# Kernel tuning notes

Measured on AMD Instinct MI355X. Metric: run time of the kernel, lower is better.

## Reference

```python
import jax, jax.numpy as jnp
import numpy as np

EMB = 256   # EMB_SIZE hard-coded in source
H = 8       # num heads (all heads share the same Q/K/V, as in source)
DK = EMB // H  # 32
B, T = 16, 2048
LN_EPS = 1e-5


def _layernorm(a, g, b):
    m = jnp.mean(a, axis=-1, keepdims=True)
    v = jnp.mean(jnp.square(a - m), axis=-1, keepdims=True)
    return (a - m) * jax.lax.rsqrt(v + LN_EPS) * g + b


def setup_inputs() -> dict:
    key = jax.random.key(0)
    ks = jax.random.split(key, 8)
    sc = 0.02
    return {
        "x": jax.random.normal(ks[0], (B, T, EMB), jnp.float32),
        "Wq": jax.random.normal(ks[1], (EMB, DK), jnp.float32) * sc,
        "Wk": jax.random.normal(ks[2], (EMB, DK), jnp.float32) * sc,
        "Wv": jax.random.normal(ks[3], (EMB, DK), jnp.float32) * sc,
        "Wp": jax.random.normal(ks[4], (EMB, EMB), jnp.float32) * sc,
        "bp": jnp.zeros((EMB,), jnp.float32),
        "W1": jax.random.normal(ks[5], (EMB, 4 * EMB), jnp.float32) * sc,
        "b1": jnp.zeros((4 * EMB,), jnp.float32),
        "W2": jax.random.normal(ks[6], (4 * EMB, EMB), jnp.float32) * sc,
        "b2": jnp.zeros((EMB,), jnp.float32),
        "g1": jnp.ones((EMB,), jnp.float32),
        "be1": jnp.zeros((EMB,), jnp.float32),
        "g2": jnp.ones((EMB,), jnp.float32),
        "be2": jnp.zeros((EMB,), jnp.float32),
    }


def reference(x, Wq, Wk, Wv, Wp, bp, W1, b1, W2, b2, g1, be1, g2, be2):
    # Single shared-head QKV projections (bias-free), as in source
    q = x @ Wq  # [B,T,DK]
    k = x @ Wk
    v = x @ Wv
    # Causal self-attention with explicit score matrix [B,T,T]
    scores = jnp.einsum("btd,bsd->bts", q, k) / jnp.sqrt(jnp.float32(DK))
    causal = jnp.tril(jnp.ones((T, T), dtype=bool))
    scores = jnp.where(causal, scores, -jnp.inf)
    a = jax.nn.softmax(scores, axis=-1)
    attn = jnp.einsum("bts,bsd->btd", a, v)  # [B,T,DK]
    # Source concatenates h identical copies of the same attention output
    cat = jnp.tile(attn, (1, 1, H))  # [B,T,EMB]
    mh = cat @ Wp + bp
    y1 = _layernorm(x + mh, g1, be1)
    ff = jax.nn.gelu(y1 @ W1 + b1, approximate=False) @ W2 + b2
    return _layernorm(y1 + ff, g2, be2)
```

## Files before the change

### kernel.cpp

```cpp
#include <hip/hip_runtime.h>

#define BB 16
#define TT 2048
#define EE 256
#define DK 32
#define MM (BB*TT)
#define FF 1024

typedef __bf16 bf16_t;
typedef __bf16 bf16x8 __attribute__((ext_vector_type(8)));
typedef __bf16 bf16x4 __attribute__((ext_vector_type(4)));
typedef float  f32x4  __attribute__((ext_vector_type(4)));

__device__ __forceinline__ f32x4 mfma16(bf16x8 a, bf16x8 b, f32x4 c){
  return __builtin_amdgcn_mfma_f32_16x16x32_bf16(a, b, c, 0, 0, 0);
}
__device__ __forceinline__ void gload_lds16(const void* g, void* l){
  __builtin_amdgcn_global_load_lds((__attribute__((address_space(1))) void*)g,
                                   (__attribute__((address_space(3))) void*)l,
                                   16, 0, 0);
}

__launch_bounds__(256)
__global__ void prep_kernel(const float* __restrict__ Wq, const float* __restrict__ Wk,
                            const float* __restrict__ Wv, const float* __restrict__ Wp,
                            const float* __restrict__ W1, const float* __restrict__ W2,
                            bf16_t* __restrict__ wqkv, bf16_t* __restrict__ wpT,
                            bf16_t* __restrict__ w1t, bf16_t* __restrict__ w2t)
{
  const int i = blockIdx.x*256 + threadIdx.x;
  if (i < 96*256) {
    const int r = i >> 8, c = i & 255;
    float v;
    if (r < 32)      v = Wq[c*32 + r] * 0.17677669529663687f;
    else if (r < 64) v = Wk[c*32 + (r-32)];
    else             v = Wv[c*32 + (r-64)];
    wqkv[i] = (bf16_t)v;
  }
  if (i < 256*32) {
    const int n = i >> 5, k = i & 31;
    float s = 0.f;
    #pragma unroll
    for (int h = 0; h < 8; ++h) s += Wp[(h*32 + k)*256 + n];
    wpT[i] = (bf16_t)s;
  }
  if (i < 1024*256) {
    const int n = i >> 8, k = i & 255;
    w1t[i] = (bf16_t)W1[(size_t)k*1024 + n];
  }
  if (i < 256*1024) {
    const int n = i >> 10, k = i & 1023;
    w2t[i] = (bf16_t)W2[(size_t)k*256 + n];
  }
}

__launch_bounds__(256)
__global__ void qkv_kernel(const float* __restrict__ x, const bf16_t* __restrict__ wqkv,
                           bf16_t* __restrict__ q, bf16_t* __restrict__ kd,
                           bf16_t* __restrict__ vT)
{
  __shared__ bf16_t Ws[96*256];
  bf16_t* Vt = Ws;
  const int tid = threadIdx.x;
  #pragma unroll
  for (int i = 0; i < 12; ++i) {
    const int v8  = tid + i*256;
    const int row = v8 >> 5;
    const int bir = (v8 & 31) * 16;
    *(bf16x8*)((char*)Ws + row*512 + (bir ^ ((row & 7) << 4))) =
        *(const bf16x8*)(wqkv + (size_t)v8*8);
  }
  __syncthreads();

  const int w = tid >> 6, l = tid & 63;
  const int lr = l & 15, lk4 = l >> 4, lkb = lk4*8;
  const int m0 = blockIdx.x * 64;
  const int arow = m0 + w*16 + lr;
  const float* xr = x + (size_t)arow * 256;

  f32x4 acc[6] = {};
  #pragma unroll
  for (int s = 0; s < 8; ++s) {
    const int kb = s*32 + lkb;
    const float4 v0 = *(const float4*)(xr + kb);
    const float4 v1 = *(const float4*)(xr + kb + 4);
    bf16x8 a;
    a[0]=(bf16_t)v0.x; a[1]=(bf16_t)v0.y; a[2]=(bf16_t)v0.z; a[3]=(bf16_t)v0.w;
    a[4]=(bf16_t)v1.x; a[5]=(bf16_t)v1.y; a[6]=(bf16_t)v1.z; a[7]=(bf16_t)v1.w;
    #pragma unroll
    for (int j = 0; j < 6; ++j) {
      const int nrow = j*16 + lr;
      const bf16x8 bf = *(const bf16x8*)((const char*)Ws + nrow*512 +
                                         ((kb*2) ^ ((nrow & 7) << 4)));
      acc[j] = mfma16(a, bf, acc[j]);
    }
  }
  #pragma unroll
  for (int j = 0; j < 4; ++j) {
    #pragma unroll
    for (int r = 0; r < 4; ++r) {
      const int orow = m0 + w*16 + lk4*4 + r;
      const int col  = j*16 + lr;
      const bf16_t v = (bf16_t)acc[j][r];
      if (col < 32) q[(size_t)orow*32 + col] = v;
      else          kd[(size_t)orow*32 + (col-32)] = v;
    }
  }
  __syncthreads();
  #pragma unroll
  for (int j = 4; j < 6; ++j)
    #pragma unroll
    for (int r = 0; r < 4; ++r) {
      const int d = (j-4)*16 + lr;
      const int t = w*16 + lk4*4 + r;
      *(bf16_t*)((char*)Vt + d*128 + ((((t>>3) ^ (d&7))<<4) | ((t&7)*2))) =
          (bf16_t)acc[j][r];
    }
  __syncthreads();
  {
    const int d = tid >> 3, c8 = tid & 7;
    const bf16x8 v = *(const bf16x8*)((char*)Vt + d*128 + ((c8 ^ (d&7))<<4));
    *(bf16x8*)(vT + ((size_t)(m0 >> 11)*32 + d)*TT + (m0 & 2047) + c8*8) = v;
  }
}

__launch_bounds__(256)
__global__ void attnp_kernel(const bf16_t* __restrict__ q, const bf16_t* __restrict__ kd,
                             const bf16_t* __restrict__ vT,
                             float* __restrict__ part_acc, float* __restrict__ part_ml)
{
  __shared__ bf16_t P[4][16*128];
  const int tid = threadIdx.x;
  const int w = tid >> 6, l = tid & 63;
  const int wv = blockIdx.x*4 + w;
  const int lr = l & 15, g4 = l >> 4;
  const float NEG_INF = -__builtin_inff();

  const int b = wv / 320;
  const int u = wv - b*320;
  int r, base;
  if      (u >= 192) { r = 3; base = 192; }
  else if (u >= 96)  { r = 2; base = 96;  }
  else if (u >= 32)  { r = 1; base = 32;  }
  else               { r = 0; base = 0;   }
  const int qq = u - base;
  const int g  = r*32 + qq / (r+1);
  const int c  = qq - (qq / (r+1))*(r+1);
  const int t_total = (g >> 3) + 1;
  const int t0 = c*4;
  const int t1 = min(t0 + 4, t_total);

  const bf16_t* qb = q  + (size_t)b*TT*32;
  const bf16_t* kb = kd + (size_t)b*TT*32;
  const bf16_t* vb = vT + (size_t)b*32*TT;
  const int q0 = g*16;
  const int qg = q0 + lr;

  const bf16x8 qa = *(const bf16x8*)(qb + (size_t)(q0 + lr)*32 + g4*8);
  const bf16_t* v0r = vb + (size_t)lr*TT;
  const bf16_t* v1r = vb + (size_t)(16 + lr)*TT;

  f32x4 acc0 = {0.f,0.f,0.f,0.f}, acc1 = {0.f,0.f,0.f,0.f};
  float mrun = NEG_INF, lsum = 0.f;
  char* pb = (char*)&P[w][0];
  const int swz = (lr & 7) << 4;
  const f32x4 zf = {0.f,0.f,0.f,0.f};

  for (int t = t0; t < t1; ++t) {
    const int k0 = t * 128;
    f32x4 s[8];
    #pragma unroll
    for (int cc = 0; cc < 8; ++cc) {
      const bf16x8 kf = *(const bf16x8*)(kb + (size_t)(k0 + cc*16 + lr)*32 + g4*8);
      s[cc] = mfma16(kf, qa, zf);
    }
    if (t == t_total - 1) {
      #pragma unroll
      for (int cc = 0; cc < 8; ++cc)
        #pragma unroll
        for (int rr = 0; rr < 4; ++rr)
          if (k0 + cc*16 + g4*4 + rr > qg) s[cc][rr] = NEG_INF;
    }
    float mt = NEG_INF;
    #pragma unroll
    for (int cc = 0; cc < 8; ++cc) {
      float a01 = fmaxf(s[cc][0], s[cc][1]), a23 = fmaxf(s[cc][2], s[cc][3]);
      mt = fmaxf(mt, fmaxf(a01, a23));
    }
    mt = fmaxf(mt, __shfl_xor(mt, 16));
    mt = fmaxf(mt, __shfl_xor(mt, 32));
    const float mn = fmaxf(mrun, mt);
    const float sc = __expf(mrun - mn);
    float ps = 0.f;
    #pragma unroll
    for (int cc = 0; cc < 8; ++cc) {
      float p0 = __expf(s[cc][0]-mn), p1 = __expf(s[cc][1]-mn);
      float p2 = __expf(s[cc][2]-mn), p3 = __expf(s[cc][3]-mn);
      s[cc][0]=p0; s[cc][1]=p1; s[cc][2]=p2; s[cc][3]=p3;
      ps += (p0+p1) + (p2+p3);
    }
    ps += __shfl_xor(ps, 16);
    ps += __shfl_xor(ps, 32);
    lsum = lsum*sc + ps;
    mrun = mn;
    acc0 *= sc; acc1 *= sc;
    #pragma unroll
    for (int cc = 0; cc < 8; ++cc) {
      bf16x4 pk;
      pk[0]=(bf16_t)s[cc][0]; pk[1]=(bf16_t)s[cc][1];
      pk[2]=(bf16_t)s[cc][2]; pk[3]=(bf16_t)s[cc][3];
      *(bf16x4*)(pb + lr*256 + ((cc*32 + g4*8) ^ swz)) = pk;
    }
    #pragma unroll
    for (int h = 0; h < 4; ++h) {
      const bf16x8 pbf = *(const bf16x8*)(pb + lr*256 + ((h*64 + g4*16) ^ swz));
      acc0 = mfma16(*(const bf16x8*)(v0r + k0 + h*32 + g4*8), pbf, acc0);
      acc1 = mfma16(*(const bf16x8*)(v1r + k0 + h*32 + g4*8), pbf, acc1);
    }
  }
  float* pa = part_acc + (size_t)wv*512;
  *(f32x4*)(pa + l*8)     = acc0;
  *(f32x4*)(pa + l*8 + 4) = acc1;
  if (l < 16) {
    part_ml[wv*32 + l]      = mrun;
    part_ml[wv*32 + 16 + l] = lsum;
  }
}

__launch_bounds__(256)
__global__ void ln1f_kernel(const float* __restrict__ part_acc,
                            const float* __restrict__ part_ml,
                            const bf16_t* __restrict__ wpT,
                            const float* __restrict__ bp, const float* __restrict__ x,
                            const float* __restrict__ g1, const float* __restrict__ be1,
                            bf16_t* __restrict__ y1b)
{
  __shared__ char SM[57344];
  char* wp_s  = SM;
  char* att_s = SM + 16384;
  float* bp_s = (float*)(SM + 20480);
  char* y_s   = SM + 24576;
  const int tid = threadIdx.x;
  const int w = tid >> 6, l = tid & 63;
  const int lr = l & 15, g4 = l >> 4;
  const float NEG_INF = -__builtin_inff();

  #pragma unroll
  for (int p = 0; p < 4; ++p) {
    const int idx = p*256 + tid;
    const int n = idx >> 2, c = idx & 3;
    gload_lds16(wpT + (size_t)n*32 + ((c ^ (n & 3)) * 8), wp_s + idx*16);
  }
  if (tid < 64) ((float4*)bp_s)[tid] = ((const float4*)bp)[tid];

  const int id = blockIdx.x*4 + w;
  const int b = id >> 7, g = id & 127;
  {
    const int rr = g >> 5;
    const int base = (rr == 0) ? 0 : (rr == 1) ? 32 : (rr == 2) ? 96 : 192;
    const int p0 = b*320 + base + (g - (rr << 5))*(rr + 1);
    const int nc = rr + 1;
    float M = NEG_INF;
    float mv0=NEG_INF, mv1=NEG_INF, mv2=NEG_INF, mv3=NEG_INF;
    float lv0=0, lv1=0, lv2=0, lv3=0;
    f32x4 a00={0,0,0,0}, a01={0,0,0,0}, a10={0,0,0,0}, a11={0,0,0,0};
    f32x4 a20={0,0,0,0}, a21={0,0,0,0}, a30={0,0,0,0}, a31={0,0,0,0};
    {
      const float* pa = part_acc + (size_t)p0*512;
      a00 = *(const f32x4*)(pa + l*8); a01 = *(const f32x4*)(pa + l*8 + 4);
      mv0 = part_ml[p0*32 + lr]; lv0 = part_ml[p0*32 + 16 + lr];
    }
    if (nc > 1) {
      const float* pa = part_acc + (size_t)(p0+1)*512;
      a10 = *(const f32x4*)(pa + l*8); a11 = *(const f32x4*)(pa + l*8 + 4);
      mv1 = part_ml[(p0+1)*32 + lr]; lv1 = part_ml[(p0+1)*32 + 16 + lr];
    }
    if (nc > 2) {
      const float* pa = part_acc + (size_t)(p0+2)*512;
      a20 = *(const f32x4*)(pa + l*8); a21 = *(const f32x4*)(pa + l*8 + 4);
      mv2 = part_ml[(p0+2)*32 + lr]; lv2 = part_ml[(p0+2)*32 + 16 + lr];
    }
    if (nc > 3) {
      const float* pa = part_acc + (size_t)(p0+3)*512;
      a30 = *(const f32x4*)(pa + l*8); a31 = *(const f32x4*)(pa + l*8 + 4);
      mv3 = part_ml[(p0+3)*32 + lr]; lv3 = part_ml[(p0+3)*32 + 16 + lr];
    }
    M = fmaxf(fmaxf(mv0, mv1), fmaxf(mv2, mv3));
    const float w0 = __expf(mv0 - M), w1 = __expf(mv1 - M);
    const float w2 = __expf(mv2 - M), w3 = __expf(mv3 - M);
    const float L = lv0*w0 + lv1*w1 + lv2*w2 + lv3*w3;
    const float inv = 1.0f / L;
    const f32x4 o0 = (a00*w0 + a10*w1 + a20*w2 + a30*w3) * inv;
    const f32x4 o1 = (a01*w0 + a11*w1 + a21*w2 + a31*w3) * inv;
    char* ab = att_s + w*1024;
    bf16x4 h0, h1;
    #pragma unroll
    for (int r = 0; r < 4; ++r) { h0[r] = (bf16_t)o0[r]; h1[r] = (bf16_t)o1[r]; }
    *(bf16x4*)(ab + lr*64 + ((g4*8)      ^ ((lr & 3) << 4))) = h0;
    *(bf16x4*)(ab + lr*64 + ((32 + g4*8) ^ ((lr & 3) << 4))) = h1;
  }
  __syncthreads();

  const char* ab = att_s + w*1024;
  const bf16x8 af = *(const bf16x8*)(ab + lr*64 + ((g4*16) ^ ((lr & 3) << 4)));
  f32x4 acc[16];
  #pragma unroll
  for (int j = 0; j < 16; ++j) {
    const int n = j*16 + lr;
    const bf16x8 bf = *(const bf16x8*)(wp_s + n*64 + ((g4*16) ^ ((n & 3) << 4)));
    acc[j] = mfma16(af, bf, f32x4{0,0,0,0});
  }

  const int row0 = b*TT + g*16;
  float bb[16];
  #pragma unroll
  for (int j = 0; j < 16; ++j) bb[j] = bp_s[j*16 + lr];
  float s1[4] = {0,0,0,0}, s2[4] = {0,0,0,0};
  #pragma unroll
  for (int j = 0; j < 16; ++j)
    #pragma unroll
    for (int r = 0; r < 4; ++r) {
      const float t = acc[j][r] + bb[j] +
                      x[(size_t)(row0 + g4*4 + r)*256 + j*16 + lr];
      acc[j][r] = t;
      s1[r] += t; s2[r] += t*t;
    }
  #pragma unroll
  for (int r = 0; r < 4; ++r) {
    #pragma unroll
    for (int m = 1; m < 16; m <<= 1) {
      s1[r] += __shfl_xor(s1[r], m); s2[r] += __shfl_xor(s2[r], m);
    }
  }
  char* yb = y_s + w*8192;
  #pragma unroll
  for (int r = 0; r < 4; ++r) {
    const float mean = s1[r] * (1.0f/256.0f);
    const float var  = s2[r] * (1.0f/256.0f) - mean*mean;
    const float rs   = rsqrtf(var + 1e-5f);
    const int mrow = g4*4 + r;
    #pragma unroll
    for (int j = 0; j < 16; ++j) {
      const int col = j*16 + lr;
      const float yv = (acc[j][r] - mean)*rs*g1[col] + be1[col];
      *(bf16_t*)(yb + mrow*512 + ((col*2) ^ ((mrow & 7) << 4))) = (bf16_t)yv;
    }
  }
  __syncthreads();
  {
    char* ybw = y_s + w*8192;
    #pragma unroll
    for (int p = 0; p < 8; ++p) {
      const int u = p*64 + l;
      const int mrow = u >> 5, c16 = u & 31;
      const bf16x8 v = *(const bf16x8*)(ybw + mrow*512 + ((c16*16) ^ ((mrow & 7) << 4)));
      *(bf16x8*)(y1b + (size_t)(row0 + mrow)*256 + c16*8) = v;
    }
  }
}

__launch_bounds__(1024)
__global__ void mlp_kernel(const bf16_t* __restrict__ y1b, const bf16_t* __restrict__ w1t,
                           const float* __restrict__ b1, const bf16_t* __restrict__ w2t,
                           const float* __restrict__ b2, const float* __restrict__ g2,
                           const float* __restrict__ be2, float* __restrict__ out)
{
  __shared__ char SM[151552];
  const int tid = threadIdx.x;
  const int w = tid >> 6, l = tid & 63;
  const int lr = l & 15, g4 = l >> 4;
  const int m0 = blockIdx.x * 128;
  const int wm  = (w >> 1) * 16;
  const int wn1 = (w & 1) * 32;
  const int wn2 = (w & 1) * 128;

  *(float*)(SM + 147456 + tid*4) = b1[tid];
  asm volatile("s_waitcnt vmcnt(0) lgkmcnt(0)" ::: "memory");
  __builtin_amdgcn_sched_barrier(0);

  #define ST_W1(i, d)                                                         \
    { _Pragma("unroll")                                                       \
      for (int p_ = 0; p_ < 2; ++p_) {                                        \
        const int idx_ = p_*1024 + tid;                                       \
        const int r_ = idx_ >> 5, c_ = idx_ & 31;                             \
        const int sc_ = (c_ & 24) | ((c_ ^ r_) & 7);                          \
        gload_lds16(w1t + (size_t)((i)*64 + r_)*256 + sc_*8,                  \
                    SM + (d)*32768 + idx_*16);                                \
      } }
  #define ST_W2(i, d)                                                         \
    { _Pragma("unroll")                                                       \
      for (int p_ = 0; p_ < 2; ++p_) {                                        \
        const int idx_ = p_*1024 + tid;                                       \
        const int r_ = idx_ >> 3, c_ = idx_ & 7;                              \
        gload_lds16(w2t + (size_t)r_*1024 + (i)*64 + ((c_ ^ r_) & 7)*8,       \
                    SM + 65536 + (d)*32768 + idx_*16);                        \
      } }

  ST_W1(0, 0);
  bf16x8 aA[8];
  #pragma unroll
  for (int kk = 0; kk < 8; ++kk)
    aA[kk] = *(const bf16x8*)(y1b + (size_t)(m0 + wm + lr)*256 + kk*32 + g4*8);
  ST_W2(0, 0);
  ST_W1(1, 1);

  f32x4 oacc[8] = {};
  char* hb = SM + 131072;

  #pragma unroll 1
  for (int i = 0; i < 16; ++i) {
    if (i < 15) { asm volatile("s_waitcnt vmcnt(4)" ::: "memory"); }
    else        { asm volatile("s_waitcnt vmcnt(2)" ::: "memory"); }
    __builtin_amdgcn_sched_barrier(0);
    __builtin_amdgcn_s_barrier();
    const char* sw1 = SM + (i & 1)*32768;
    f32x4 ah0 = {0.f,0.f,0.f,0.f}, ah1 = {0.f,0.f,0.f,0.f};
    __builtin_amdgcn_s_setprio(1);
    #pragma unroll
    for (int kk = 0; kk < 8; ++kk) {
      const int off = kk*64 + g4*16;
      const int n0r = wn1 + lr, n1r = wn1 + 16 + lr;
      const bf16x8 bf0 = *(const bf16x8*)(sw1 + n0r*512 + (off ^ ((n0r & 7) << 4)));
      const bf16x8 bf1 = *(const bf16x8*)(sw1 + n1r*512 + (off ^ ((n1r & 7) << 4)));
      ah0 = mfma16(aA[kk], bf0, ah0);
      ah1 = mfma16(aA[kk], bf1, ah1);
    }
    __builtin_amdgcn_s_setprio(0);
    #pragma unroll
    for (int j = 0; j < 2; ++j) {
      const float bias = *(const float*)(SM + 147456 + (i*64 + wn1 + j*16 + lr)*4);
      const f32x4 av = j ? ah1 : ah0;
      const int hcol2 = (wn1 + j*16 + lr)*2;
      #pragma unroll
      for (int r = 0; r < 4; ++r) {
        const int hrow = wm + g4*4 + r;
        const float v = av[r] + bias;
        const float z = 1.5957691216057308f * v * fmaf(0.044715f, v*v, 1.0f);
        const float gg = v * __builtin_amdgcn_rcpf(1.0f + __expf(-z));
        *(bf16_t*)(hb + hrow*128 + (hcol2 ^ ((hrow & 7) << 4))) = (bf16_t)gg;
      }
    }
    asm volatile("s_waitcnt lgkmcnt(0)" ::: "memory");
    __builtin_amdgcn_sched_barrier(0);
    if (i < 15) { asm volatile("s_waitcnt vmcnt(2)" ::: "memory"); }
    else        { asm volatile("s_waitcnt vmcnt(0)" ::: "memory"); }
    __builtin_amdgcn_sched_barrier(0);
    __builtin_amdgcn_s_barrier();
    const char* sw2 = SM + 65536 + (i & 1)*32768;
    __builtin_amdgcn_s_setprio(1);
    #pragma unroll
    for (int kk2 = 0; kk2 < 2; ++kk2) {
      const int off = kk2*64 + g4*16;
      const int hr = wm + lr;
      const bf16x8 ha = *(const bf16x8*)(hb + hr*128 + (off ^ ((hr & 7) << 4)));
      #pragma unroll
      for (int j3 = 0; j3 < 8; ++j3) {
        const int n = wn2 + j3*16 + lr;
        const bf16x8 wb = *(const bf16x8*)(sw2 + n*128 + (off ^ ((n & 7) << 4)));
        oacc[j3] = mfma16(ha, wb, oacc[j3]);
      }
    }
    __builtin_amdgcn_s_setprio(0);
    if (i < 15) ST_W2(i+1, (i+1)&1);
    if (i < 14) ST_W1(i+2, i&1);
  }
  #undef ST_W1
  #undef ST_W2

  float b2r[8], g2r[8], be2r[8];
  #pragma unroll
  for (int j3 = 0; j3 < 8; ++j3) {
    const int col = wn2 + j3*16 + lr;
    b2r[j3] = b2[col]; g2r[j3] = g2[col]; be2r[j3] = be2[col];
  }
  #pragma unroll
  for (int r = 0; r < 4; ++r) {
    const int grow = m0 + wm + g4*4 + r;
    #pragma unroll
    for (int j3 = 0; j3 < 8; ++j3) {
      const int col = wn2 + j3*16 + lr;
      oacc[j3][r] += b2r[j3] + (float)y1b[(size_t)grow*256 + col];
    }
  }
  __syncthreads();
  float* red = (float*)SM;
  #pragma unroll
  for (int r = 0; r < 4; ++r) {
    float s1 = 0.f, s2 = 0.f;
    #pragma unroll
    for (int j3 = 0; j3 < 8; ++j3) { s1 += oacc[j3][r]; s2 += oacc[j3][r]*oacc[j3][r]; }
    #pragma unroll
    for (int m = 1; m < 16; m <<= 1) { s1 += __shfl_xor(s1, m); s2 += __shfl_xor(s2, m); }
    if (lr == 0) {
      const int rl = wm + g4*4 + r;
      red[rl*4 + (w & 1)*2]     = s1;
      red[rl*4 + (w & 1)*2 + 1] = s2;
    }
  }
  __syncthreads();
  #pragma unroll
  for (int r = 0; r < 4; ++r) {
    const int rl = wm + g4*4 + r;
    const float S1 = red[rl*4+0] + red[rl*4+2];
    const float S2 = red[rl*4+1] + red[rl*4+3];
    const float mean = S1 * (1.0f/256.0f);
    const float var  = S2 * (1.0f/256.0f) - mean*mean;
    const float rs   = rsqrtf(var + 1e-5f);
    #pragma unroll
    for (int j3 = 0; j3 < 8; ++j3) {
      const int col = wn2 + j3*16 + lr;
      out[(size_t)(m0 + rl)*256 + col] = (oacc[j3][r] - mean)*rs*g2r[j3] + be2r[j3];
    }
  }
}

extern "C" void kernel_launch(void* const* d_in, const int* in_sizes, int n_in,
                              void* d_out, int out_size, void* d_ws, size_t ws_size,
                              hipStream_t stream)
{
  const float* x   = (const float*)d_in[0];
  const float* Wq  = (const float*)d_in[1];
  const float* Wk  = (const float*)d_in[2];
  const float* Wv  = (const float*)d_in[3];
  const float* Wp  = (const float*)d_in[4];
  const float* bp  = (const float*)d_in[5];
  const float* W1  = (const float*)d_in[6];
  const float* b1  = (const float*)d_in[7];
  const float* W2  = (const float*)d_in[8];
  const float* b2  = (const float*)d_in[9];
  const float* g1  = (const float*)d_in[10];
  const float* be1 = (const float*)d_in[11];
  const float* g2  = (const float*)d_in[12];
  const float* be2 = (const float*)d_in[13];

  char* ws = (char*)d_ws;
  bf16_t* qd   = (bf16_t*)(ws + ((size_t)0  << 20));
  bf16_t* kd   = (bf16_t*)(ws + ((size_t)2  << 20));
  bf16_t* vTd  = (bf16_t*)(ws + ((size_t)4  << 20));
  bf16_t* y1b  = (bf16_t*)(ws + ((size_t)8  << 20));
  bf16_t* wqkv = (bf16_t*)(ws + ((size_t)24 << 20));
  bf16_t* wpT  = (bf16_t*)(ws + ((size_t)25 << 20));
  bf16_t* w1t  = (bf16_t*)(ws + ((size_t)26 << 20));
  bf16_t* w2t  = (bf16_t*)(ws + ((size_t)27 << 20));
  float*  pml  = (float*) (ws + ((size_t)28 << 20));
  float*  pacc = (float*) (ws + ((size_t)29 << 20));
  float* out = (float*)d_out;

  prep_kernel<<<1024, 256, 0, stream>>>(Wq, Wk, Wv, Wp, W1, W2, wqkv, wpT, w1t, w2t);
  qkv_kernel<<<512, 256, 0, stream>>>(x, wqkv, qd, kd, vTd);
  attnp_kernel<<<1280, 256, 0, stream>>>(qd, kd, vTd, pacc, pml);
  ln1f_kernel<<<512, 256, 0, stream>>>(pacc, pml, wpT, bp, x, g1, be1, y1b);
  mlp_kernel<<<256, 1024, 0, stream>>>(y1b, w1t, b1, w2t, b2, g2, be2, out);
}
```

Baseline: 123.2 us.

## Warp-specialize MLP kernel into producer GEMM1 and consumer GEMM2 warp groups

Restructures the fused MLP kernel so that 8 waves compute the first GEMM plus GELU on 32-wide hidden chunks and write them into a double-buffered LDS tile. The other 8 waves consume the previous chunk for the second GEMM and then run the final LayerNorm. This is meant to overlap the two GEMM stages. Shared memory also drops from about 148KB to 84KB, and the launch bounds now request more occupancy. The trade-offs are a barrier every chunk with a full vmcnt(0) wait, smaller chunks (33 iterations instead of 16), and half the waves idle during each phase.

```diff
diff --git a/kernel.cpp b/kernel.cpp
--- a/kernel.cpp
+++ b/kernel.cpp
@@ -260,7 +260,6 @@
     const int base = (rr == 0) ? 0 : (rr == 1) ? 32 : (rr == 2) ? 96 : 192;
     const int p0 = b*320 + base + (g - (rr << 5))*(rr + 1);
     const int nc = rr + 1;
-    float M = NEG_INF;
     float mv0=NEG_INF, mv1=NEG_INF, mv2=NEG_INF, mv3=NEG_INF;
     float lv0=0, lv1=0, lv2=0, lv3=0;
     f32x4 a00={0,0,0,0}, a01={0,0,0,0}, a10={0,0,0,0}, a11={0,0,0,0};
@@ -285,7 +284,7 @@
       a30 = *(const f32x4*)(pa + l*8); a31 = *(const f32x4*)(pa + l*8 + 4);
       mv3 = part_ml[(p0+3)*32 + lr]; lv3 = part_ml[(p0+3)*32 + 16 + lr];
     }
-    M = fmaxf(fmaxf(mv0, mv1), fmaxf(mv2, mv3));
+    const float M = fmaxf(fmaxf(mv0, mv1), fmaxf(mv2, mv3));
     const float w0 = __expf(mv0 - M), w1 = __expf(mv1 - M);
     const float w2 = __expf(mv2 - M), w3 = __expf(mv3 - M);
     const float L = lv0*w0 + lv1*w1 + lv2*w2 + lv3*w3;
@@ -359,159 +358,182 @@
   }
 }
 
-__launch_bounds__(1024)
+__launch_bounds__(1024, 4)
 __global__ void mlp_kernel(const bf16_t* __restrict__ y1b, const bf16_t* __restrict__ w1t,
                            const float* __restrict__ b1, const bf16_t* __restrict__ w2t,
                            const float* __restrict__ b2, const float* __restrict__ g2,
                            const float* __restrict__ be2, float* __restrict__ out)
 {
-  __shared__ char SM[151552];
+  __shared__ char SM[86016];
+  char* W1b = SM;
+  char* W2b = SM + 32768;
+  char* hb  = SM + 65536;
+  float* b1s = (float*)(SM + 81920);
   const int tid = threadIdx.x;
   const int w = tid >> 6, l = tid & 63;
   const int lr = l & 15, g4 = l >> 4;
   const int m0 = blockIdx.x * 128;
-  const int wm  = (w >> 1) * 16;
-  const int wn1 = (w & 1) * 32;
-  const int wn2 = (w & 1) * 128;
-
-  *(float*)(SM + 147456 + tid*4) = b1[tid];
-  asm volatile("s_waitcnt vmcnt(0) lgkmcnt(0)" ::: "memory");
-  __builtin_amdgcn_sched_barrier(0);
-
-  #define ST_W1(i, d)                                                         \
-    { _Pragma("unroll")                                                       \
-      for (int p_ = 0; p_ < 2; ++p_) {                                        \
-        const int idx_ = p_*1024 + tid;                                       \
-        const int r_ = idx_ >> 5, c_ = idx_ & 31;                             \
-        const int sc_ = (c_ & 24) | ((c_ ^ r_) & 7);                          \
-        gload_lds16(w1t + (size_t)((i)*64 + r_)*256 + sc_*8,                  \
-                    SM + (d)*32768 + idx_*16);                                \
-      } }
-  #define ST_W2(i, d)                                                         \
-    { _Pragma("unroll")                                                       \
-      for (int p_ = 0; p_ < 2; ++p_) {                                        \
-        const int idx_ = p_*1024 + tid;                                       \
-        const int r_ = idx_ >> 3, c_ = idx_ & 7;                              \
-        gload_lds16(w2t + (size_t)r_*1024 + (i)*64 + ((c_ ^ r_) & 7)*8,       \
-                    SM + 65536 + (d)*32768 + idx_*16);                        \
-      } }
-
-  ST_W1(0, 0);
-  bf16x8 aA[8];
-  #pragma unroll
-  for (int kk = 0; kk < 8; ++kk)
-    aA[kk] = *(const bf16x8*)(y1b + (size_t)(m0 + wm + lr)*256 + kk*32 + g4*8);
-  ST_W2(0, 0);
-  ST_W1(1, 1);
-
-  f32x4 oacc[8] = {};
-  char* hb = SM + 131072;
-
-  #pragma unroll 1
-  for (int i = 0; i < 16; ++i) {
-    if (i < 15) { asm volatile("s_waitcnt vmcnt(4)" ::: "memory"); }
-    else        { asm volatile("s_waitcnt vmcnt(2)" ::: "memory"); }
+
+  b1s[tid] = b1[tid];
+
+  #define ST_W1(c, s)                                                         \
+    { const int r_ = tid >> 5, c5_ = tid & 31;                                \
+      const int sc_ = (c5_ & 24) | ((c5_ ^ r_) & 7);                          \
+      gload_lds16(w1t + (size_t)((c)*32 + r_)*256 + sc_*8,                    \
+                  W1b + (s)*16384 + tid*16); }
+  #define ST_W2(c, s)                                                         \
+    { const int r_ = tid >> 2, c2_ = tid & 3;                                 \
+      gload_lds16(w2t + (size_t)r_*1024 + (c)*32 + ((c2_ ^ r_) & 3)*8,        \
+                  W2b + (s)*16384 + tid*16); }
+
+  if (w < 8) {
+    const int rwp = w & 3, cwp = w >> 2;
+    const int mb = rwp*32;
+    bf16x8 aA[2][8];
+    #pragma unroll
+    for (int t = 0; t < 2; ++t)
+      #pragma unroll
+      for (int kk = 0; kk < 8; ++kk)
+        aA[t][kk] = *(const bf16x8*)(y1b +
+            (size_t)(m0 + mb + t*16 + lr)*256 + kk*32 + g4*8);
+    asm volatile("s_waitcnt vmcnt(0) lgkmcnt(0)" ::: "memory");
     __builtin_amdgcn_sched_barrier(0);
-    __builtin_amdgcn_s_barrier();
-    const char* sw1 = SM + (i & 1)*32768;
-    f32x4 ah0 = {0.f,0.f,0.f,0.f}, ah1 = {0.f,0.f,0.f,0.f};
-    __builtin_amdgcn_s_setprio(1);
-    #pragma unroll
-    for (int kk = 0; kk < 8; ++kk) {
-      const int off = kk*64 + g4*16;
-      const int n0r = wn1 + lr, n1r = wn1 + 16 + lr;
-      const bf16x8 bf0 = *(const bf16x8*)(sw1 + n0r*512 + (off ^ ((n0r & 7) << 4)));
-      const bf16x8 bf1 = *(const bf16x8*)(sw1 + n1r*512 + (off ^ ((n1r & 7) << 4)));
-      ah0 = mfma16(aA[kk], bf0, ah0);
-      ah1 = mfma16(aA[kk], bf1, ah1);
-    }
-    __builtin_amdgcn_s_setprio(0);
-    #pragma unroll
-    for (int j = 0; j < 2; ++j) {
-      const float bias = *(const float*)(SM + 147456 + (i*64 + wn1 + j*16 + lr)*4);
-      const f32x4 av = j ? ah1 : ah0;
-      const int hcol2 = (wn1 + j*16 + lr)*2;
+    ST_W1(0, 0);
+    const int nr = cwp*16 + lr;
+    const int hcol2 = (cwp*16 + lr)*2;
+    #pragma unroll 1
+    for (int i = 0; i <= 32; ++i) {
+      asm volatile("s_waitcnt vmcnt(0)" ::: "memory");
+      __builtin_amdgcn_sched_barrier(0);
+      __builtin_amdgcn_s_barrier();
+      __builtin_amdgcn_sched_barrier(0);
+      if (i < 31) ST_W1(i+1, (i+1)&1);
+      if (i < 32) ST_W2(i, i&1);
+      if (i < 32) {
+        const char* sw1 = W1b + (i & 1)*16384;
+        f32x4 ah[2] = {};
+        __builtin_amdgcn_s_setprio(1);
+        #pragma unroll
+        for (int kk = 0; kk < 8; ++kk) {
+          const bf16x8 bf = *(const bf16x8*)(sw1 + nr*512 +
+                                             ((kk*64 + g4*16) ^ ((nr & 7) << 4)));
+          ah[0] = mfma16(aA[0][kk], bf, ah[0]);
+          ah[1] = mfma16(aA[1][kk], bf, ah[1]);
+        }
+        __builtin_amdgcn_s_setprio(0);
+        const float bias = b1s[i*32 + cwp*16 + lr];
+        char* hw = hb + (i & 1)*8192;
+        #pragma unroll
+        for (int t = 0; t < 2; ++t)
+          #pragma unroll
+          for (int r = 0; r < 4; ++r) {
+            const int m = mb + t*16 + g4*4 + r;
+            const float v = ah[t][r] + bias;
+            const float z = 1.5957691216057308f * v * fmaf(0.044715f, v*v, 1.0f);
+            const float gg = v * __builtin_amdgcn_rcpf(1.0f + __expf(-z));
+            *(bf16_t*)(hw + m*64 + (hcol2 ^ ((m & 3) << 4))) = (bf16_t)gg;
+          }
+        asm volatile("s_waitcnt lgkmcnt(0)" ::: "memory");
+        __builtin_amdgcn_sched_barrier(0);
+      }
+    }
+    __syncthreads();
+    __syncthreads();
+  } else {
+    const int c = w - 8;
+    const int rwc = c & 3, cwc = c >> 2;
+    const int mb = rwc*32, nb = cwc*128;
+    asm volatile("s_waitcnt vmcnt(0) lgkmcnt(0)" ::: "memory");
+    __builtin_amdgcn_sched_barrier(0);
+    ST_W1(0, 0);
+    f32x4 oacc[2][8] = {};
+    #pragma unroll 1
+    for (int i = 0; i <= 32; ++i) {
+      asm volatile("s_waitcnt vmcnt(0)" ::: "memory");
+      __builtin_amdgcn_sched_barrier(0);
+      __builtin_amdgcn_s_barrier();
+      __builtin_amdgcn_sched_barrier(0);
+      if (i < 31) ST_W1(i+1, (i+1)&1);
+      if (i < 32) ST_W2(i, i&1);
+      if (i > 0) {
+        const char* sw2 = W2b + ((i-1) & 1)*16384;
+        const char* hs  = hb  + ((i-1) & 1)*8192;
+        bf16x8 ha[2], wb[8];
+        __builtin_amdgcn_s_setprio(1);
+        #pragma unroll
+        for (int i3 = 0; i3 < 2; ++i3) {
+          const int row = mb + i3*16 + lr;
+          ha[i3] = *(const bf16x8*)(hs + row*64 + ((g4*16) ^ ((row & 3) << 4)));
+        }
+        #pragma unroll
+        for (int j3 = 0; j3 < 8; ++j3) {
+          const int n = nb + j3*16 + lr;
+          wb[j3] = *(const bf16x8*)(sw2 + n*64 + ((g4*16) ^ ((n & 3) << 4)));
+        }
+        #pragma unroll
+        for (int i3 = 0; i3 < 2; ++i3)
+          #pragma unroll
+          for (int j3 = 0; j3 < 8; ++j3)
+            oacc[i3][j3] = mfma16(ha[i3], wb[j3], oacc[i3][j3]);
+        __builtin_amdgcn_s_setprio(0);
+      }
+    }
+    float b2r[8], g2r[8], be2r[8];
+    #pragma unroll
+    for (int j3 = 0; j3 < 8; ++j3) {
+      const int col = nb + j3*16 + lr;
+      b2r[j3] = b2[col]; g2r[j3] = g2[col]; be2r[j3] = be2[col];
+    }
+    #pragma unroll
+    for (int i3 = 0; i3 < 2; ++i3)
       #pragma unroll
       for (int r = 0; r < 4; ++r) {
-        const int hrow = wm + g4*4 + r;
-        const float v = av[r] + bias;
-        const float z = 1.5957691216057308f * v * fmaf(0.044715f, v*v, 1.0f);
-        const float gg = v * __builtin_amdgcn_rcpf(1.0f + __expf(-z));
-        *(bf16_t*)(hb + hrow*128 + (hcol2 ^ ((hrow & 7) << 4))) = (bf16_t)gg;
+        const int grow = m0 + mb + i3*16 + g4*4 + r;
+        #pragma unroll
+        for (int j3 = 0; j3 < 8; ++j3) {
+          const int col = nb + j3*16 + lr;
+          oacc[i3][j3][r] += b2r[j3] + (float)y1b[(size_t)grow*256 + col];
+        }
       }
-    }
-    asm volatile("s_waitcnt lgkmcnt(0)" ::: "memory");
-    __builtin_amdgcn_sched_barrier(0);
-    if (i < 15) { asm volatile("s_waitcnt vmcnt(2)" ::: "memory"); }
-    else        { asm volatile("s_waitcnt vmcnt(0)" ::: "memory"); }
-    __builtin_amdgcn_sched_barrier(0);
-    __builtin_amdgcn_s_barrier();
-    const char* sw2 = SM + 65536 + (i & 1)*32768;
-    __builtin_amdgcn_s_setprio(1);
-    #pragma unroll
-    for (int kk2 = 0; kk2 < 2; ++kk2) {
-      const int off = kk2*64 + g4*16;
-      const int hr = wm + lr;
-      const bf16x8 ha = *(const bf16x8*)(hb + hr*128 + (off ^ ((hr & 7) << 4)));
+    __syncthreads();
+    float* red = (float*)SM;
+    #pragma unroll
+    for (int i3 = 0; i3 < 2; ++i3)
       #pragma unroll
-      for (int j3 = 0; j3 < 8; ++j3) {
-        const int n = wn2 + j3*16 + lr;
-        const bf16x8 wb = *(const bf16x8*)(sw2 + n*128 + (off ^ ((n & 7) << 4)));
-        oacc[j3] = mfma16(ha, wb, oacc[j3]);
+      for (int r = 0; r < 4; ++r) {
+        float s1 = 0.f, s2 = 0.f;
+        #pragma unroll
+        for (int j3 = 0; j3 < 8; ++j3) {
+          s1 += oacc[i3][j3][r]; s2 += oacc[i3][j3][r]*oacc[i3][j3][r];
+        }
+        #pragma unroll
+        for (int m = 1; m < 16; m <<= 1) { s1 += __shfl_xor(s1, m); s2 += __shfl_xor(s2, m); }
+        if (lr == 0) {
+          const int rl = mb + i3*16 + g4*4 + r;
+          red[rl*4 + cwc*2]     = s1;
+          red[rl*4 + cwc*2 + 1] = s2;
+        }
       }
-    }
-    __builtin_amdgcn_s_setprio(0);
-    if (i < 15) ST_W2(i+1, (i+1)&1);
-    if (i < 14) ST_W1(i+2, i&1);
+    __syncthreads();
+    #pragma unroll
+    for (int i3 = 0; i3 < 2; ++i3)
+      #pragma unroll
+      for (int r = 0; r < 4; ++r) {
+        const int rl = mb + i3*16 + g4*4 + r;
+        const float S1 = red[rl*4+0] + red[rl*4+2];
+        const float S2 = red[rl*4+1] + red[rl*4+3];
+        const float mean = S1 * (1.0f/256.0f);
+        const float var  = S2 * (1.0f/256.0f) - mean*mean;
+        const float rs   = rsqrtf(var + 1e-5f);
+        #pragma unroll
+        for (int j3 = 0; j3 < 8; ++j3) {
+          const int col = nb + j3*16 + lr;
+          out[(size_t)(m0 + rl)*256 + col] = (oacc[i3][j3][r] - mean)*rs*g2r[j3] + be2r[j3];
+        }
+      }
   }
   #undef ST_W1
   #undef ST_W2
-
-  float b2r[8], g2r[8], be2r[8];
-  #pragma unroll
-  for (int j3 = 0; j3 < 8; ++j3) {
-    const int col = wn2 + j3*16 + lr;
-    b2r[j3] = b2[col]; g2r[j3] = g2[col]; be2r[j3] = be2[col];
-  }
-  #pragma unroll
-  for (int r = 0; r < 4; ++r) {
-    const int grow = m0 + wm + g4*4 + r;
-    #pragma unroll
-    for (int j3 = 0; j3 < 8; ++j3) {
-      const int col = wn2 + j3*16 + lr;
-      oacc[j3][r] += b2r[j3] + (float)y1b[(size_t)grow*256 + col];
-    }
-  }
-  __syncthreads();
-  float* red = (float*)SM;
-  #pragma unroll
-  for (int r = 0; r < 4; ++r) {
-    float s1 = 0.f, s2 = 0.f;
-    #pragma unroll
-    for (int j3 = 0; j3 < 8; ++j3) { s1 += oacc[j3][r]; s2 += oacc[j3][r]*oacc[j3][r]; }
-    #pragma unroll
-    for (int m = 1; m < 16; m <<= 1) { s1 += __shfl_xor(s1, m); s2 += __shfl_xor(s2, m); }
-    if (lr == 0) {
-      const int rl = wm + g4*4 + r;
-      red[rl*4 + (w & 1)*2]     = s1;
-      red[rl*4 + (w & 1)*2 + 1] = s2;
-    }
-  }
-  __syncthreads();
-  #pragma unroll
-  for (int r = 0; r < 4; ++r) {
-    const int rl = wm + g4*4 + r;
-    const float S1 = red[rl*4+0] + red[rl*4+2];
-    const float S2 = red[rl*4+1] + red[rl*4+3];
-    const float mean = S1 * (1.0f/256.0f);
-    const float var  = S2 * (1.0f/256.0f) - mean*mean;
-    const float rs   = rsqrtf(var + 1e-5f);
-    #pragma unroll
-    for (int j3 = 0; j3 < 8; ++j3) {
-      const int col = wn2 + j3*16 + lr;
-      out[(size_t)(m0 + rl)*256 + col] = (oacc[j3][r] - mean)*rs*g2r[j3] + be2r[j3];
-    }
-  }
 }
 
 extern "C" void kernel_launch(void* const* d_in, const int* in_sizes, int n_in,
```

Result: slower. 137.1 us (+11.2%).
